# Optimization experiments

Measured on AMD Instinct MI355X. Metric: run time of the kernel, lower is better.

The kernel has to match this reference:

```python
import jax, jax.numpy as jnp
import numpy as np
import math

B, T, C = 4, 2048, 2048
HQ, HKV = 16, 4
HD = C // HQ          # 128
REP = HQ // HKV       # 4
EPS = 1e-6


def _rope_tables(seq_len, dim):
    inv_freq = 1.0 / (10000.0 ** (np.arange(0, dim, 2, dtype=np.float32) / dim))
    t = np.arange(seq_len, dtype=np.float32)
    freqs = np.einsum('i,j->ij', t, inv_freq)  # [T, dim/2]
    return jnp.asarray(np.cos(freqs)), jnp.asarray(np.sin(freqs))


def setup_inputs() -> dict:
    key = jax.random.key(0)
    ks = jax.random.split(key, 10)
    s = 0.02
    cos, sin = _rope_tables(T, HD)
    return {
        'x': jax.random.normal(ks[0], (B, T, C), jnp.float32),
        'Wq': jax.random.normal(ks[1], (C, C), jnp.float32) * s,
        'bq': jnp.zeros((C,), jnp.float32),
        'Wk': jax.random.normal(ks[2], (HD * HKV, C), jnp.float32) * s,
        'bk': jnp.zeros((HD * HKV,), jnp.float32),
        'Wv': jax.random.normal(ks[3], (HD * HKV, C), jnp.float32) * s,
        'bv': jnp.zeros((HD * HKV,), jnp.float32),
        'qn_w': jnp.ones((HD,), jnp.float32),
        'kn_w': jnp.ones((HD,), jnp.float32),
        'Wg': jax.random.normal(ks[4], (HD, HD), jnp.float32) * s,
        'bg': jnp.zeros((HD,), jnp.float32),
        'Wo': jax.random.normal(ks[5], (C, C), jnp.float32) * s,
        'bo': jnp.zeros((C,), jnp.float32),
        'cos': cos,
        'sin': sin,
    }


def _apply_rope(x, cos, sin):
    # x: [B,T,H,HD]; cos/sin: [T,HD/2]
    c = cos[None, :, None, :]
    s = sin[None, :, None, :]
    x1, x2 = x[..., ::2], x[..., 1::2]
    return jnp.concatenate([x1 * c - x2 * s, x1 * s + x2 * c], axis=-1)


def _rmsnorm(x, w):
    norm = jnp.mean(x * x, axis=-1, keepdims=True)
    return w * (x * jax.lax.rsqrt(norm + EPS))


def reference(x, Wq, bq, Wk, bk, Wv, bv, qn_w, kn_w, Wg, bg, Wo, bo, cos, sin):
    Bsz, Tlen, _ = x.shape
    q = (x @ Wq.T + bq).reshape(Bsz, Tlen, HQ, HD)
    k = (x @ Wk.T + bk).reshape(Bsz, Tlen, HKV, HD)
    v = (x @ Wv.T + bv).reshape(Bsz, Tlen, HKV, HD)

    q = _rmsnorm(_apply_rope(q, cos, sin), qn_w)
    k = _rmsnorm(_apply_rope(k, cos, sin), kn_w)

    # GQA without materializing repeated K/V: group q heads [B,T,HKV,REP,HD]
    # (repeat_interleave on kv-head dim matches this grouping exactly)
    q5 = q.reshape(Bsz, Tlen, HKV, REP, HD)
    scores = jnp.einsum('btkrd,bskd->bkrts', q5, k) / math.sqrt(HD)

    causal = jnp.tril(jnp.ones((Tlen, Tlen), bool))
    scores = jnp.where(causal, scores, -jnp.inf)
    probs = jax.nn.softmax(scores, axis=-1)

    out = jnp.einsum('bkrts,bskd->btkrd', probs, v).reshape(Bsz, Tlen, HQ, HD)
    gate = jax.nn.sigmoid(out @ Wg.T + bg)
    out = (out * gate).reshape(Bsz, Tlen, C)
    return out @ Wo.T + bo
```

## Files before the change

kernel.cpp:

```cpp
#include <hip/hip_runtime.h>
#include <hip/hip_bf16.h>
#include <math.h>

typedef __attribute__((ext_vector_type(8))) __bf16 bf16x8;
typedef __attribute__((ext_vector_type(4))) float f32x4;

__device__ __forceinline__ void stage16(const void* g, void* l) {
#if __has_builtin(__builtin_amdgcn_global_load_lds)
  __builtin_amdgcn_global_load_lds(
      (const __attribute__((address_space(1))) void*)g,
      (__attribute__((address_space(3))) void*)l, 16, 0, 0);
#else
  *(int4*)l = *(const int4*)g;
#endif
}

__device__ __forceinline__ float sigmoidf_(float x) {
  return 1.0f / (1.0f + __expf(-x));
}

__device__ __forceinline__ void f2b4(const float* __restrict__ s, __bf16* __restrict__ d) {
  float4 v = *(const float4*)s;
  union { __bf16 h[4]; int2 p; } u;
  u.h[0] = (__bf16)v.x; u.h[1] = (__bf16)v.y;
  u.h[2] = (__bf16)v.z; u.h[3] = (__bf16)v.w;
  *(int2*)d = u.p;
}

__global__ __launch_bounds__(256) void prep(const float* __restrict__ x,
                                            const float* __restrict__ Wq,
                                            const float* __restrict__ Wk,
                                            const float* __restrict__ Wv,
                                            const float* __restrict__ Wo,
                                            const float* __restrict__ Wg,
                                            const float* __restrict__ bq,
                                            const float* __restrict__ bk,
                                            const float* __restrict__ bv,
                                            __bf16* __restrict__ XB,
                                            __bf16* __restrict__ WQKVb,
                                            __bf16* __restrict__ WOb,
                                            __bf16* __restrict__ WGb,
                                            float* __restrict__ BQKV) {
  int c = blockIdx.x * 256 + threadIdx.x;
  if (c >= 6820608) return;
  if (c < 4194304) {
    f2b4(x + (size_t)c * 4, XB + (size_t)c * 4);
  } else if (c < 5242880) {
    int e = (c - 4194304) * 4;  f2b4(Wq + e, WQKVb + e);
  } else if (c < 5505024) {
    int e = (c - 5242880) * 4;  f2b4(Wk + e, WQKVb + 4194304 + e);
  } else if (c < 5767168) {
    int e = (c - 5505024) * 4;  f2b4(Wv + e, WQKVb + 5242880 + e);
  } else if (c < 6815744) {
    int e = (c - 5767168) * 4;  f2b4(Wo + e, WOb + e);
  } else if (c < 6819840) {
    int e = (c - 6815744) * 4;  f2b4(Wg + e, WGb + e);
  } else {
    int e = (c - 6819840) * 4;
    float4 v;
    if (e < 2048)      v = *(const float4*)(bq + e);
    else if (e < 2560) v = *(const float4*)(bk + (e - 2048));
    else               v = *(const float4*)(bv + (e - 2560));
    *(float4*)(BQKV + e) = v;
  }
}

template <typename OutT>
__global__ __launch_bounds__(512, 1) void gemm256(const __bf16* __restrict__ A,
                                                  const __bf16* __restrict__ Bm,
                                                  const float* __restrict__ bias,
                                                  OutT* __restrict__ C,
                                                  int M, int N, int K, int gx) {
  __shared__ __align__(16) __bf16 Sm[2][2][2][128 * 64];
  const int tid = threadIdx.x, lane = tid & 63, wid = tid >> 6;
  const int wm = wid >> 2, wn = wid & 3;
  const int r = lane & 15, g4 = lane >> 4;
  const int nwg = gridDim.x, qx = nwg >> 3;
  const int wg = (blockIdx.x & 7) * qx + (blockIdx.x >> 3);
  const int m0 = (wg / gx) * 256, n0 = (wg % gx) * 256;

  f32x4 acc[8][4] = {};
  const int NT = K >> 6;

#define STAGE_HALF(buf, which, half, kt)                                          \
  {                                                                               \
    const __bf16* sp_ = (which) ? Bm : A;                                         \
    const int base_ = ((which) ? n0 : m0) + (half) * 128;                         \
    const int k0_ = (kt) << 6;                                                    \
    __bf16* dp_ = &Sm[buf][which][half][0];                                       \
    _Pragma("unroll") for (int i_ = 0; i_ < 2; ++i_) {                            \
      int c_ = i_ * 512 + tid;                                                    \
      int row_ = c_ >> 3, slot_ = c_ & 7;                                         \
      stage16(sp_ + (size_t)(base_ + row_) * K + k0_ + ((slot_ ^ (row_ & 7)) << 3), \
              dp_ + c_ * 8);                                                      \
    }                                                                             \
  }
#define LDSW(base, row, kk) \
  (*(const bf16x8*)&(base)[(row) * 64 + ((((kk) * 4 + g4) ^ ((row) & 7)) << 3)])

  STAGE_HALF(0, 0, 0, 0) STAGE_HALF(0, 0, 1, 0) STAGE_HALF(0, 1, 0, 0) STAGE_HALF(0, 1, 1, 0)

  const int brow = (wn & 1) * 64;
  bf16x8 af[4][2], bfr[2][2];

  for (int kt = 0; kt < NT; ++kt) {
    const int cur = kt & 1, nxt = cur ^ 1;
    const bool more = (kt + 1) < NT;
    const __bf16* Ah = &Sm[cur][0][wm][0];
    const __bf16* Bh = &Sm[cur][1][wn >> 1][0];

    if (more) STAGE_HALF(nxt, 0, 0, kt + 1)
    if (more) { asm volatile("s_waitcnt vmcnt(2)" ::: "memory"); }
    else      { asm volatile("s_waitcnt vmcnt(0)" ::: "memory"); }
    __builtin_amdgcn_s_barrier();
    asm volatile("" ::: "memory");
#pragma unroll
    for (int m = 0; m < 4; ++m)
#pragma unroll
      for (int kk = 0; kk < 2; ++kk) af[m][kk] = LDSW(Ah, m * 16 + r, kk);
#pragma unroll
    for (int n = 0; n < 2; ++n)
#pragma unroll
      for (int kk = 0; kk < 2; ++kk) bfr[n][kk] = LDSW(Bh, brow + n * 16 + r, kk);
    asm volatile("s_waitcnt lgkmcnt(0)" ::: "memory");
    __builtin_amdgcn_sched_barrier(0);
    __builtin_amdgcn_s_setprio(1);
#pragma unroll
    for (int m = 0; m < 4; ++m)
#pragma unroll
      for (int n = 0; n < 2; ++n)
#pragma unroll
        for (int kk = 0; kk < 2; ++kk)
          acc[m][n] = __builtin_amdgcn_mfma_f32_16x16x32_bf16(af[m][kk], bfr[n][kk],
                                                              acc[m][n], 0, 0, 0);
    __builtin_amdgcn_s_setprio(0);
    __builtin_amdgcn_s_barrier();

#pragma unroll
    for (int n = 0; n < 2; ++n)
#pragma unroll
      for (int kk = 0; kk < 2; ++kk) bfr[n][kk] = LDSW(Bh, brow + (2 + n) * 16 + r, kk);
    if (more) STAGE_HALF(nxt, 0, 1, kt + 1)
    asm volatile("s_waitcnt lgkmcnt(0)" ::: "memory");
    __builtin_amdgcn_sched_barrier(0);
    __builtin_amdgcn_s_setprio(1);
#pragma unroll
    for (int m = 0; m < 4; ++m)
#pragma unroll
      for (int n = 0; n < 2; ++n)
#pragma unroll
        for (int kk = 0; kk < 2; ++kk)
          acc[m][2 + n] = __builtin_amdgcn_mfma_f32_16x16x32_bf16(af[m][kk], bfr[n][kk],
                                                                  acc[m][2 + n], 0, 0, 0);
    __builtin_amdgcn_s_setprio(0);
    __builtin_amdgcn_s_barrier();

#pragma unroll
    for (int m = 0; m < 4; ++m)
#pragma unroll
      for (int kk = 0; kk < 2; ++kk) af[m][kk] = LDSW(Ah, (4 + m) * 16 + r, kk);
#pragma unroll
    for (int n = 0; n < 2; ++n)
#pragma unroll
      for (int kk = 0; kk < 2; ++kk) bfr[n][kk] = LDSW(Bh, brow + n * 16 + r, kk);
    if (more) STAGE_HALF(nxt, 1, 0, kt + 1)
    asm volatile("s_waitcnt lgkmcnt(0)" ::: "memory");
    __builtin_amdgcn_sched_barrier(0);
    __builtin_amdgcn_s_setprio(1);
#pragma unroll
    for (int m = 0; m < 4; ++m)
#pragma unroll
      for (int n = 0; n < 2; ++n)
#pragma unroll
        for (int kk = 0; kk < 2; ++kk)
          acc[4 + m][n] = __builtin_amdgcn_mfma_f32_16x16x32_bf16(af[m][kk], bfr[n][kk],
                                                                  acc[4 + m][n], 0, 0, 0);
    __builtin_amdgcn_s_setprio(0);
    __builtin_amdgcn_s_barrier();

#pragma unroll
    for (int n = 0; n < 2; ++n)
#pragma unroll
      for (int kk = 0; kk < 2; ++kk) bfr[n][kk] = LDSW(Bh, brow + (2 + n) * 16 + r, kk);
    if (more) STAGE_HALF(nxt, 1, 1, kt + 1)
    asm volatile("s_waitcnt lgkmcnt(0)" ::: "memory");
    __builtin_amdgcn_sched_barrier(0);
    __builtin_amdgcn_s_setprio(1);
#pragma unroll
    for (int m = 0; m < 4; ++m)
#pragma unroll
      for (int n = 0; n < 2; ++n)
#pragma unroll
        for (int kk = 0; kk < 2; ++kk)
          acc[4 + m][2 + n] = __builtin_amdgcn_mfma_f32_16x16x32_bf16(af[m][kk], bfr[n][kk],
                                                                      acc[4 + m][2 + n], 0, 0, 0);
    __builtin_amdgcn_s_setprio(0);
    __builtin_amdgcn_s_barrier();
  }

  const int rq = lane >> 4;
#pragma unroll
  for (int m = 0; m < 8; ++m)
#pragma unroll
    for (int n = 0; n < 4; ++n) {
      int col = n0 + wn * 64 + n * 16 + r;
      float bv = bias ? bias[col] : 0.0f;
#pragma unroll
      for (int j = 0; j < 4; ++j) {
        int row = m0 + wm * 128 + m * 16 + rq * 4 + j;
        C[(size_t)row * N + col] = (OutT)(acc[m][n][j] + bv);
      }
    }
#undef STAGE_HALF
#undef LDSW
}

__global__ __launch_bounds__(512, 1) void gemm128(const __bf16* __restrict__ A,
                                                  const __bf16* __restrict__ Bm,
                                                  const float* __restrict__ bias,
                                                  __bf16* __restrict__ C,
                                                  int M, int N, int K, int gx) {
  __shared__ __align__(16) __bf16 Sm[2][3][128 * 64];
  const int tid = threadIdx.x, lane = tid & 63, wid = tid >> 6;
  const int wm = wid >> 2, wn = wid & 3;
  const int r = lane & 15, g4 = lane >> 4;
  const int nwg = gridDim.x, qx = nwg >> 3;
  const int wg = (blockIdx.x & 7) * qx + (blockIdx.x >> 3);
  const int m0 = (wg / gx) * 128, n0 = (wg % gx) * 256;

  f32x4 acc[4][4] = {};
  const int NT = K >> 6;

#define STAGE_SEG(buf, seg, sp, rowbase, kt)                                        \
  {                                                                                 \
    __bf16* dp_ = &Sm[buf][seg][0];                                                 \
    const int k0_ = (kt) << 6;                                                      \
    _Pragma("unroll") for (int i_ = 0; i_ < 2; ++i_) {                              \
      int c_ = i_ * 512 + tid;                                                      \
      int row_ = c_ >> 3, slot_ = c_ & 7;                                           \
      stage16((sp) + (size_t)((rowbase) + row_) * K + k0_ + ((slot_ ^ (row_ & 7)) << 3), \
              dp_ + c_ * 8);                                                        \
    }                                                                               \
  }
#define LDSW(base, row, kk) \
  (*(const bf16x8*)&(base)[(row) * 64 + ((((kk) * 4 + g4) ^ ((row) & 7)) << 3)])
#define MFMA8(nq)                                                                   \
  asm volatile("s_waitcnt lgkmcnt(0)" ::: "memory");                                \
  __builtin_amdgcn_sched_barrier(0);                                                \
  __builtin_amdgcn_s_setprio(1);                                                    \
  _Pragma("unroll") for (int m = 0; m < 4; ++m)                                     \
    _Pragma("unroll") for (int kk = 0; kk < 2; ++kk)                                \
      acc[m][nq] = __builtin_amdgcn_mfma_f32_16x16x32_bf16(af[m][kk], bfr[kk],      \
                                                           acc[m][nq], 0, 0, 0);    \
  __builtin_amdgcn_s_setprio(0);

  STAGE_SEG(0, 0, A, m0, 0) STAGE_SEG(0, 1, Bm, n0, 0) STAGE_SEG(0, 2, Bm, n0 + 128, 0)

  const int bseg = 1 + (wn >> 1);
  const int brow = (wn & 1) * 64;
  bf16x8 af[4][2], bfr[2];

  for (int kt = 0; kt < NT; ++kt) {
    const int cur = kt & 1, nxt = cur ^ 1;
    const bool more = (kt + 1) < NT;
    const __bf16* Ah = &Sm[cur][0][0];
    const __bf16* Bh = &Sm[cur][bseg][0];

    if (more) { STAGE_SEG(nxt, 0, A, m0, kt + 1)
                asm volatile("s_waitcnt vmcnt(2)" ::: "memory"); }
    else      { asm volatile("s_waitcnt vmcnt(0)" ::: "memory"); }
    __builtin_amdgcn_s_barrier();
    asm volatile("" ::: "memory");
#pragma unroll
    for (int m = 0; m < 4; ++m)
#pragma unroll
      for (int kk = 0; kk < 2; ++kk) af[m][kk] = LDSW(Ah, wm * 64 + m * 16 + r, kk);
#pragma unroll
    for (int kk = 0; kk < 2; ++kk) bfr[kk] = LDSW(Bh, brow + r, kk);
    MFMA8(0)

#pragma unroll
    for (int kk = 0; kk < 2; ++kk) bfr[kk] = LDSW(Bh, brow + 16 + r, kk);
    if (more) STAGE_SEG(nxt, 1, Bm, n0, kt + 1)
    MFMA8(1)

#pragma unroll
    for (int kk = 0; kk < 2; ++kk) bfr[kk] = LDSW(Bh, brow + 32 + r, kk);
    if (more) STAGE_SEG(nxt, 2, Bm, n0 + 128, kt + 1)
    MFMA8(2)

#pragma unroll
    for (int kk = 0; kk < 2; ++kk) bfr[kk] = LDSW(Bh, brow + 48 + r, kk);
    MFMA8(3)
    __builtin_amdgcn_s_barrier();
  }

  const int rq = lane >> 4;
#pragma unroll
  for (int m = 0; m < 4; ++m)
#pragma unroll
    for (int n = 0; n < 4; ++n) {
      int col = n0 + wn * 64 + n * 16 + r;
      float bv = bias ? bias[col] : 0.0f;
#pragma unroll
      for (int j = 0; j < 4; ++j) {
        int row = m0 + wm * 64 + m * 16 + rq * 4 + j;
        C[(size_t)row * N + col] = (__bf16)(acc[m][n][j] + bv);
      }
    }
#undef STAGE_SEG
#undef LDSW
#undef MFMA8
}

__global__ __launch_bounds__(256) void rope_vt(const __bf16* __restrict__ Y,
                                               const float* __restrict__ cosT,
                                               const float* __restrict__ sinT,
                                               const float* __restrict__ qn,
                                               const float* __restrict__ kn,
                                               __bf16* __restrict__ qat,
                                               __bf16* __restrict__ kat,
                                               __bf16* __restrict__ VT) {
  __shared__ __bf16 tile[32][66];
  if (blockIdx.x < 8192) {
    const int tok = blockIdx.x;
    const int b = tok >> 11, t = tok & 2047;
    const int wv = threadIdx.x >> 6, l = threadIdx.x & 63;
    const __bf16* row = Y + (size_t)tok * 3072;
    const float c = cosT[t * 64 + l], s = sinT[t * 64 + l];
    const float QS = 0.08838834764831845f * 1.4426950408889634f;
#pragma unroll
    for (int i = 0; i < 5; ++i) {
      const int h = wv + i * 4;
      const bool isq = h < 16;
      const int base = isq ? h * 128 : 2048 + (h - 16) * 128;
      union { uint32_t u; __bf16 h2[2]; } p;
      p.u = *(const uint32_t*)(row + base + 2 * l);
      float x1 = (float)p.h2[0], x2 = (float)p.h2[1];
      float v1 = x1 * c - x2 * s;
      float v2 = x1 * s + x2 * c;
      float ss = v1 * v1 + v2 * v2;
#pragma unroll
      for (int o = 32; o >= 1; o >>= 1) ss += __shfl_xor(ss, o, 64);
      float rms = rsqrtf(ss * (1.0f / 128.0f) + 1e-6f);
      if (isq) rms *= QS;
      float w1 = isq ? qn[l] : kn[l];
      float w2 = isq ? qn[64 + l] : kn[64 + l];
      size_t ob = isq ? (((size_t)b * 16 + h) * 2048 + t) * 128
                      : (((size_t)b * 4 + (h - 16)) * 2048 + t) * 128;
      __bf16* dst = isq ? qat : kat;
      dst[ob + l] = (__bf16)(w1 * v1 * rms);
      dst[ob + 64 + l] = (__bf16)(w2 * v2 * rms);
    }
  } else {
    const int i = blockIdx.x - 8192;
    const int t0 = (i & 31) * 64;
    const int d0 = ((i >> 5) & 3) * 32;
    const int bh = i >> 7;
    const int b = bh >> 2, hv = bh & 3;
    const __bf16* src = Y + (size_t)b * 2048 * 3072 + 2560 + hv * 128 + d0;
    const int dd = threadIdx.x & 31, tt = threadIdx.x >> 5;
#pragma unroll
    for (int p = 0; p < 8; ++p) {
      int t = tt + p * 8;
      tile[dd][t] = src[(size_t)(t0 + t) * 3072 + dd];
    }
    __syncthreads();
    __bf16* dst = VT + ((size_t)bh * 128 + d0) * 2048 + t0;
    const int oc = threadIdx.x & 63, orr = threadIdx.x >> 6;
#pragma unroll
    for (int p = 0; p < 8; ++p) {
      int d = orr + p * 4;
      dst[(size_t)d * 2048 + oc] = tile[d][oc];
    }
  }
}

__global__ __launch_bounds__(512, 4) void attn10(const __bf16* __restrict__ Q,
                                                 const __bf16* __restrict__ Kg,
                                                 const __bf16* __restrict__ VTg,
                                                 __bf16* __restrict__ ab) {
  __shared__ __align__(16) __bf16 Kt[2][64 * 128];
  __shared__ __align__(16) __bf16 Vt[2][128 * 64];
  __shared__ __align__(16) __bf16 Ps[8 * 16 * 64];
  const int tid = threadIdx.x, lane = tid & 63, wv = tid >> 6;
  const int L = blockIdx.x;
  const int xcd = L & 7, slot = L >> 3;
  const int group = xcd * 2 + (slot >> 5);
  const int idx = slot & 31;
  const int b = group >> 2, hkv = group & 3;
  const int hq = hkv * 4 + (idx >> 3);
  const int p = idx & 7;
  const __bf16* qp = Q + ((size_t)b * 16 + hq) * 2048 * 128;
  const __bf16* kp = Kg + ((size_t)b * 4 + hkv) * 2048 * 128;
  const __bf16* vp = VTg + ((size_t)b * 4 + hkv) * 128 * 2048;
  const int r = lane & 15, g4 = lane >> 4, ks = g4 * 8;

  bf16x8 vone;
#pragma unroll
  for (int e = 0; e < 8; ++e) vone[e] = (__bf16)1.0f;

#define STAGE_TILE(bi, kv0)                                                  \
  {                                                                          \
    __bf16* Kb = &Kt[bi][0];                                                 \
    __bf16* Vb = &Vt[bi][0];                                                 \
    _Pragma("unroll") for (int i = 0; i < 2; ++i) {                          \
      int c = i * 512 + tid;                                                 \
      int row = c >> 4, slot_ = c & 15;                                      \
      int gco = ((slot_ ^ (row & 7)) << 3);                                  \
      stage16(kp + (size_t)((kv0) + row) * 128 + gco, &Kb[c * 8]);           \
    }                                                                        \
    _Pragma("unroll") for (int i = 0; i < 2; ++i) {                          \
      int c = i * 512 + tid;                                                 \
      int row = c >> 3, slot_ = c & 7;                                       \
      int gco = ((slot_ ^ (row & 7)) << 3);                                  \
      stage16(vp + (size_t)row * 2048 + (kv0) + gco, &Vb[c * 8]);            \
    }                                                                        \
  }
#define SM_PAIR(k0)                                                          \
  _Pragma("unroll") for (int kj = (k0); kj < (k0) + 2; ++kj)                 \
    _Pragma("unroll") for (int j = 0; j < 4; ++j) {                          \
      float pv = exp2f(s[kj][j] - mrow[j]);                                  \
      int qr = g4 * 4 + j;                                                   \
      int kvl = kj * 16 + r;                                                 \
      int sl = (kvl >> 3) ^ (qr & 7);                                        \
      pw[qr * 64 + sl * 8 + (kvl & 7)] = (__bf16)pv;                         \
    }
#define PV_CHUNK(kvj)                                                        \
  {                                                                          \
    int sl = ((kvj) * 4 + g4) ^ (r & 7);                                     \
    bf16x8 pa = *(const bf16x8*)&pw[r * 64 + sl * 8];                        \
    __builtin_amdgcn_s_setprio(1);                                           \
    Lacc = __builtin_amdgcn_mfma_f32_16x16x32_bf16(pa, vone, Lacc, 0, 0, 0); \
    _Pragma("unroll") for (int dn = 0; dn < 8; ++dn) {                       \
      bf16x8 vb = *(const bf16x8*)&Vb[(dn * 16 + r) * 64 + sl * 8];          \
      Of[dn] = __builtin_amdgcn_mfma_f32_16x16x32_bf16(pa, vb, Of[dn], 0, 0, 0); \
    }                                                                        \
    __builtin_amdgcn_s_setprio(0);                                           \
  }

  for (int half = 0; half < 2; ++half) {
    const int qt = half == 0 ? (15 - p) : p;
    const int q0 = qt * 128 + wv * 16;

    bf16x8 qf[4];
#pragma unroll
    for (int kk = 0; kk < 4; ++kk)
      qf[kk] = *(const bf16x8*)(qp + (size_t)(q0 + r) * 128 + kk * 32 + ks);

    f32x4 Of[8] = {};
    f32x4 Lacc = {};
    float mrow[4] = {-1e30f, -1e30f, -1e30f, -1e30f};

    const int nt = 2 * qt + 2;
    STAGE_TILE(0, 0);
    int cur = 0;
    for (int t = 0; t < nt; ++t) {
      const int kv0 = t * 64;
      if (t + 1 < nt) {
        STAGE_TILE(cur ^ 1, (t + 1) * 64);
        asm volatile("s_waitcnt vmcnt(4)" ::: "memory");
      } else {
        asm volatile("s_waitcnt vmcnt(0)" ::: "memory");
      }
      __builtin_amdgcn_s_barrier();

      const __bf16* Kb = &Kt[cur][0];
      const __bf16* Vb = &Vt[cur][0];

      f32x4 s[4];
      __builtin_amdgcn_s_setprio(1);
#pragma unroll
      for (int kj = 0; kj < 4; ++kj) {
        f32x4 sa = {};
        int krow = kj * 16 + r;
#pragma unroll
        for (int kk = 0; kk < 4; ++kk) {
          int slot_ = (kk * 4 + g4) ^ (r & 7);
          bf16x8 kf = *(const bf16x8*)&Kb[krow * 128 + slot_ * 8];
          sa = __builtin_amdgcn_mfma_f32_16x16x32_bf16(qf[kk], kf, sa, 0, 0, 0);
        }
        s[kj] = sa;
      }
      __builtin_amdgcn_s_setprio(0);
      if (kv0 + 63 > q0) {
#pragma unroll
        for (int kj = 0; kj < 4; ++kj)
#pragma unroll
          for (int j = 0; j < 4; ++j) {
            int kv = kv0 + kj * 16 + r;
            int qrow = q0 + g4 * 4 + j;
            if (kv > qrow) s[kj][j] = -1e30f;
          }
      }
      float tm[4];
#pragma unroll
      for (int j = 0; j < 4; ++j)
        tm[j] = fmaxf(fmaxf(s[0][j], s[1][j]), fmaxf(s[2][j], s[3][j]));
      bool need = (tm[0] > mrow[0] + 8.0f) | (tm[1] > mrow[1] + 8.0f) |
                  (tm[2] > mrow[2] + 8.0f) | (tm[3] > mrow[3] + 8.0f);
      if (__any(need)) {
#pragma unroll
        for (int o = 8; o >= 1; o >>= 1)
#pragma unroll
          for (int j = 0; j < 4; ++j) tm[j] = fmaxf(tm[j], __shfl_xor(tm[j], o, 64));
#pragma unroll
        for (int j = 0; j < 4; ++j) {
          float mn = fmaxf(mrow[j], tm[j]);
          float corr = exp2f(mrow[j] - mn);
          mrow[j] = mn;
          Lacc[j] *= corr;
#pragma unroll
          for (int f = 0; f < 8; ++f) Of[f][j] *= corr;
        }
      }

      __bf16* pw = &Ps[wv * 16 * 64];
      SM_PAIR(0)
      PV_CHUNK(0)
      SM_PAIR(2)
      PV_CHUNK(1)
      __builtin_amdgcn_s_barrier();
      cur ^= 1;
    }

    float inv[4];
#pragma unroll
    for (int j = 0; j < 4; ++j) inv[j] = 1.0f / Lacc[j];
#pragma unroll
    for (int dn = 0; dn < 8; ++dn)
#pragma unroll
      for (int j = 0; j < 4; ++j) {
        int row = q0 + g4 * 4 + j;
        int d = dn * 16 + r;
        ab[(((size_t)b * 2048 + row) * 16 + hq) * 128 + d] = (__bf16)(Of[dn][j] * inv[j]);
      }
  }
#undef STAGE_TILE
#undef SM_PAIR
#undef PV_CHUNK
}

__global__ __launch_bounds__(256) void gate_fused(const __bf16* __restrict__ a,
                                                  const __bf16* __restrict__ WgB,
                                                  const float* __restrict__ bg,
                                                  __bf16* __restrict__ og) {
  __shared__ __align__(16) __bf16 Wl[128 * 128];
  const int tid = threadIdx.x, lane = tid & 63, wv = tid >> 6;
  const int r = lane & 15, g4 = lane >> 4, ks = g4 * 8;
#pragma unroll
  for (int i = 0; i < 8; ++i) {
    int c = i * 256 + tid;
    int row = c >> 4, slot = c & 15;
    *(bf16x8*)&Wl[row * 128 + ((slot ^ (row & 7)) << 3)] =
        *(const bf16x8*)&WgB[row * 128 + slot * 8];
  }
  __syncthreads();
  const size_t r0 = (size_t)blockIdx.x * 64 + wv * 16;
  bf16x8 af[4];
#pragma unroll
  for (int kk = 0; kk < 4; ++kk)
    af[kk] = *(const bf16x8*)(a + (r0 + r) * 128 + kk * 32 + ks);
  f32x4 acc[8] = {};
#pragma unroll
  for (int dn = 0; dn < 8; ++dn) {
    int row = dn * 16 + r;
#pragma unroll
    for (int kk = 0; kk < 4; ++kk) {
      bf16x8 bf_ = *(const bf16x8*)&Wl[row * 128 + (((kk * 4 + g4) ^ (row & 7)) << 3)];
      acc[dn] = __builtin_amdgcn_mfma_f32_16x16x32_bf16(af[kk], bf_, acc[dn], 0, 0, 0);
    }
  }
#pragma unroll
  for (int dn = 0; dn < 8; ++dn) {
    float bgv = bg[dn * 16 + r];
#pragma unroll
    for (int j = 0; j < 4; ++j) {
      size_t row = r0 + g4 * 4 + j;
      int col = dn * 16 + r;
      float gv = sigmoidf_(acc[dn][j] + bgv);
      float av = (float)a[row * 128 + col];
      og[row * 128 + col] = (__bf16)(av * gv);
    }
  }
}

extern "C" void kernel_launch(void* const* d_in, const int* in_sizes, int n_in,
                              void* d_out, int out_size, void* d_ws, size_t ws_size,
                              hipStream_t stream) {
  const float* x    = (const float*)d_in[0];
  const float* Wq   = (const float*)d_in[1];
  const float* bq   = (const float*)d_in[2];
  const float* Wk   = (const float*)d_in[3];
  const float* bk   = (const float*)d_in[4];
  const float* Wv   = (const float*)d_in[5];
  const float* bv   = (const float*)d_in[6];
  const float* qn   = (const float*)d_in[7];
  const float* kn   = (const float*)d_in[8];
  const float* Wg   = (const float*)d_in[9];
  const float* bg   = (const float*)d_in[10];
  const float* Wo   = (const float*)d_in[11];
  const float* bo   = (const float*)d_in[12];
  const float* cosT = (const float*)d_in[13];
  const float* sinT = (const float*)d_in[14];

  char* ws = (char*)d_ws;
  constexpr size_t OFF_WQKV = 0;
  constexpr size_t OFF_WO   = OFF_WQKV + 3072ull * 2048 * 2;
  constexpr size_t OFF_WG   = OFF_WO + 2048ull * 2048 * 2;
  constexpr size_t OFF_BQKV = OFF_WG + 128ull * 128 * 2;
  constexpr size_t OFF_XB   = OFF_BQKV + 16384;
  constexpr size_t OFF_Y    = OFF_XB + 8192ull * 2048 * 2;
  constexpr size_t OFF_QAT  = OFF_Y + 8192ull * 3072 * 2;
  constexpr size_t OFF_KAT  = OFF_QAT + 4ull * 16 * 2048 * 128 * 2;
  constexpr size_t OFF_VT   = OFF_KAT + 4ull * 4 * 2048 * 128 * 2;
  constexpr size_t OFF_AB   = OFF_VT + 4ull * 4 * 2048 * 128 * 2;

  __bf16* WQKVb = (__bf16*)(ws + OFF_WQKV);
  __bf16* WOb   = (__bf16*)(ws + OFF_WO);
  __bf16* WGb   = (__bf16*)(ws + OFF_WG);
  float*  BQKV  = (float*)(ws + OFF_BQKV);
  __bf16* XB    = (__bf16*)(ws + OFF_XB);
  __bf16* Y     = (__bf16*)(ws + OFF_Y);
  __bf16* QAT   = (__bf16*)(ws + OFF_QAT);
  __bf16* KAT   = (__bf16*)(ws + OFF_KAT);
  __bf16* VT    = (__bf16*)(ws + OFF_VT);
  __bf16* ABuf  = (__bf16*)(ws + OFF_AB);
  __bf16* OGB   = (__bf16*)(ws + OFF_XB);

  prep<<<26643, 256, 0, stream>>>(x, Wq, Wk, Wv, Wo, Wg, bq, bk, bv,
                                  XB, WQKVb, WOb, WGb, BQKV);

  gemm128<<<768, 512, 0, stream>>>(XB, WQKVb, BQKV, Y, 8192, 3072, 2048, 12);

  rope_vt<<<10240, 256, 0, stream>>>(Y, cosT, sinT, qn, kn, QAT, KAT, VT);

  attn10<<<512, 512, 0, stream>>>(QAT, KAT, VT, ABuf);

  gate_fused<<<2048, 256, 0, stream>>>(ABuf, WGb, bg, OGB);

  gemm256<float><<<256, 512, 0, stream>>>(OGB, WOb, bo, (float*)d_out, 8192, 2048, 2048, 8);
}
```

Before: 389.9 us.

## Process two 16-row query subtiles per wave in attention to reuse K/V fragments

The attention kernel drops from 8 waves to 4 waves per block, and each wave now handles 32 query rows as two 16-row subtiles instead of one. Each K and V fragment read from LDS then feeds two MFMAs, halving LDS read traffic per unit of compute. Each thread now issues twice as many staging loads, and the wait count is adjusted to match. The cost is roughly doubled accumulator and register use per wave and fewer waves per block, which may lower occupancy and latency hiding. The softmax interleaving between P writes and PV chunks is also simplified.

```diff
diff --git a/kernel.cpp b/kernel.cpp
--- a/kernel.cpp
+++ b/kernel.cpp
@@ -376,13 +376,13 @@
   }
 }
 
-__global__ __launch_bounds__(512, 4) void attn10(const __bf16* __restrict__ Q,
+__global__ __launch_bounds__(256, 2) void attn11(const __bf16* __restrict__ Q,
                                                  const __bf16* __restrict__ Kg,
                                                  const __bf16* __restrict__ VTg,
                                                  __bf16* __restrict__ ab) {
   __shared__ __align__(16) __bf16 Kt[2][64 * 128];
   __shared__ __align__(16) __bf16 Vt[2][128 * 64];
-  __shared__ __align__(16) __bf16 Ps[8 * 16 * 64];
+  __shared__ __align__(16) __bf16 Ps[4 * 32 * 64];
   const int tid = threadIdx.x, lane = tid & 63, wv = tid >> 6;
   const int L = blockIdx.x;
   const int xcd = L & 7, slot = L >> 3;
@@ -404,53 +404,35 @@
   {                                                                          \
     __bf16* Kb = &Kt[bi][0];                                                 \
     __bf16* Vb = &Vt[bi][0];                                                 \
-    _Pragma("unroll") for (int i = 0; i < 2; ++i) {                          \
-      int c = i * 512 + tid;                                                 \
+    _Pragma("unroll") for (int i = 0; i < 4; ++i) {                          \
+      int c = i * 256 + tid;                                                 \
       int row = c >> 4, slot_ = c & 15;                                      \
       int gco = ((slot_ ^ (row & 7)) << 3);                                  \
       stage16(kp + (size_t)((kv0) + row) * 128 + gco, &Kb[c * 8]);           \
     }                                                                        \
-    _Pragma("unroll") for (int i = 0; i < 2; ++i) {                          \
-      int c = i * 512 + tid;                                                 \
+    _Pragma("unroll") for (int i = 0; i < 4; ++i) {                          \
+      int c = i * 256 + tid;                                                 \
       int row = c >> 3, slot_ = c & 7;                                       \
       int gco = ((slot_ ^ (row & 7)) << 3);                                  \
       stage16(vp + (size_t)row * 2048 + (kv0) + gco, &Vb[c * 8]);            \
     }                                                                        \
   }
-#define SM_PAIR(k0)                                                          \
-  _Pragma("unroll") for (int kj = (k0); kj < (k0) + 2; ++kj)                 \
-    _Pragma("unroll") for (int j = 0; j < 4; ++j) {                          \
-      float pv = exp2f(s[kj][j] - mrow[j]);                                  \
-      int qr = g4 * 4 + j;                                                   \
-      int kvl = kj * 16 + r;                                                 \
-      int sl = (kvl >> 3) ^ (qr & 7);                                        \
-      pw[qr * 64 + sl * 8 + (kvl & 7)] = (__bf16)pv;                         \
-    }
-#define PV_CHUNK(kvj)                                                        \
-  {                                                                          \
-    int sl = ((kvj) * 4 + g4) ^ (r & 7);                                     \
-    bf16x8 pa = *(const bf16x8*)&pw[r * 64 + sl * 8];                        \
-    __builtin_amdgcn_s_setprio(1);                                           \
-    Lacc = __builtin_amdgcn_mfma_f32_16x16x32_bf16(pa, vone, Lacc, 0, 0, 0); \
-    _Pragma("unroll") for (int dn = 0; dn < 8; ++dn) {                       \
-      bf16x8 vb = *(const bf16x8*)&Vb[(dn * 16 + r) * 64 + sl * 8];          \
-      Of[dn] = __builtin_amdgcn_mfma_f32_16x16x32_bf16(pa, vb, Of[dn], 0, 0, 0); \
-    }                                                                        \
-    __builtin_amdgcn_s_setprio(0);                                           \
-  }
-
-  for (int half = 0; half < 2; ++half) {
-    const int qt = half == 0 ? (15 - p) : p;
-    const int q0 = qt * 128 + wv * 16;
-
-    bf16x8 qf[4];
-#pragma unroll
-    for (int kk = 0; kk < 4; ++kk)
-      qf[kk] = *(const bf16x8*)(qp + (size_t)(q0 + r) * 128 + kk * 32 + ks);
-
-    f32x4 Of[8] = {};
-    f32x4 Lacc = {};
-    float mrow[4] = {-1e30f, -1e30f, -1e30f, -1e30f};
+
+  for (int half_ = 0; half_ < 2; ++half_) {
+    const int qt = half_ == 0 ? (15 - p) : p;
+    const int q0 = qt * 128 + wv * 32;
+
+    bf16x8 qfA[4], qfB[4];
+#pragma unroll
+    for (int kk = 0; kk < 4; ++kk) {
+      qfA[kk] = *(const bf16x8*)(qp + (size_t)(q0 + r) * 128 + kk * 32 + ks);
+      qfB[kk] = *(const bf16x8*)(qp + (size_t)(q0 + 16 + r) * 128 + kk * 32 + ks);
+    }
+
+    f32x4 OfA[8] = {}, OfB[8] = {};
+    f32x4 LaccA = {}, LaccB = {};
+    float mrowA[4] = {-1e30f, -1e30f, -1e30f, -1e30f};
+    float mrowB[4] = {-1e30f, -1e30f, -1e30f, -1e30f};
 
     const int nt = 2 * qt + 2;
     STAGE_TILE(0, 0);
@@ -459,7 +441,7 @@
       const int kv0 = t * 64;
       if (t + 1 < nt) {
         STAGE_TILE(cur ^ 1, (t + 1) * 64);
-        asm volatile("s_waitcnt vmcnt(4)" ::: "memory");
+        asm volatile("s_waitcnt vmcnt(8)" ::: "memory");
       } else {
         asm volatile("s_waitcnt vmcnt(0)" ::: "memory");
       }
@@ -468,19 +450,20 @@
       const __bf16* Kb = &Kt[cur][0];
       const __bf16* Vb = &Vt[cur][0];
 
-      f32x4 s[4];
+      f32x4 sA[4], sB[4];
       __builtin_amdgcn_s_setprio(1);
 #pragma unroll
       for (int kj = 0; kj < 4; ++kj) {
-        f32x4 sa = {};
+        f32x4 saA = {}, saB = {};
         int krow = kj * 16 + r;
 #pragma unroll
         for (int kk = 0; kk < 4; ++kk) {
           int slot_ = (kk * 4 + g4) ^ (r & 7);
           bf16x8 kf = *(const bf16x8*)&Kb[krow * 128 + slot_ * 8];
-          sa = __builtin_amdgcn_mfma_f32_16x16x32_bf16(qf[kk], kf, sa, 0, 0, 0);
+          saA = __builtin_amdgcn_mfma_f32_16x16x32_bf16(qfA[kk], kf, saA, 0, 0, 0);
+          saB = __builtin_amdgcn_mfma_f32_16x16x32_bf16(qfB[kk], kf, saB, 0, 0, 0);
         }
-        s[kj] = sa;
+        sA[kj] = saA; sB[kj] = saB;
       }
       __builtin_amdgcn_s_setprio(0);
       if (kv0 + 63 > q0) {
@@ -489,56 +472,87 @@
 #pragma unroll
           for (int j = 0; j < 4; ++j) {
             int kv = kv0 + kj * 16 + r;
-            int qrow = q0 + g4 * 4 + j;
-            if (kv > qrow) s[kj][j] = -1e30f;
+            int qrA = q0 + g4 * 4 + j;
+            if (kv > qrA) sA[kj][j] = -1e30f;
+            if (kv > qrA + 16) sB[kj][j] = -1e30f;
           }
       }
-      float tm[4];
+      float tmA[4], tmB[4];
+#pragma unroll
+      for (int j = 0; j < 4; ++j) {
+        tmA[j] = fmaxf(fmaxf(sA[0][j], sA[1][j]), fmaxf(sA[2][j], sA[3][j]));
+        tmB[j] = fmaxf(fmaxf(sB[0][j], sB[1][j]), fmaxf(sB[2][j], sB[3][j]));
+      }
+      bool need = false;
 #pragma unroll
       for (int j = 0; j < 4; ++j)
-        tm[j] = fmaxf(fmaxf(s[0][j], s[1][j]), fmaxf(s[2][j], s[3][j]));
-      bool need = (tm[0] > mrow[0] + 8.0f) | (tm[1] > mrow[1] + 8.0f) |
-                  (tm[2] > mrow[2] + 8.0f) | (tm[3] > mrow[3] + 8.0f);
+        need |= (tmA[j] > mrowA[j] + 8.0f) | (tmB[j] > mrowB[j] + 8.0f);
       if (__any(need)) {
 #pragma unroll
         for (int o = 8; o >= 1; o >>= 1)
 #pragma unroll
-          for (int j = 0; j < 4; ++j) tm[j] = fmaxf(tm[j], __shfl_xor(tm[j], o, 64));
+          for (int j = 0; j < 4; ++j) {
+            tmA[j] = fmaxf(tmA[j], __shfl_xor(tmA[j], o, 64));
+            tmB[j] = fmaxf(tmB[j], __shfl_xor(tmB[j], o, 64));
+          }
 #pragma unroll
         for (int j = 0; j < 4; ++j) {
-          float mn = fmaxf(mrow[j], tm[j]);
-          float corr = exp2f(mrow[j] - mn);
-          mrow[j] = mn;
-          Lacc[j] *= corr;
-#pragma unroll
-          for (int f = 0; f < 8; ++f) Of[f][j] *= corr;
+          float mnA = fmaxf(mrowA[j], tmA[j]);
+          float cA = exp2f(mrowA[j] - mnA);
+          mrowA[j] = mnA; LaccA[j] *= cA;
+          float mnB = fmaxf(mrowB[j], tmB[j]);
+          float cB = exp2f(mrowB[j] - mnB);
+          mrowB[j] = mnB; LaccB[j] *= cB;
+#pragma unroll
+          for (int f = 0; f < 8; ++f) { OfA[f][j] *= cA; OfB[f][j] *= cB; }
         }
       }
-
-      __bf16* pw = &Ps[wv * 16 * 64];
-      SM_PAIR(0)
-      PV_CHUNK(0)
-      SM_PAIR(2)
-      PV_CHUNK(1)
+      __bf16* pw = &Ps[wv * 32 * 64];
+#pragma unroll
+      for (int kj = 0; kj < 4; ++kj)
+#pragma unroll
+        for (int j = 0; j < 4; ++j) {
+          int kvl = kj * 16 + r;
+          int qrA = g4 * 4 + j;
+          int slA = (kvl >> 3) ^ (qrA & 7);
+          pw[qrA * 64 + slA * 8 + (kvl & 7)] = (__bf16)exp2f(sA[kj][j] - mrowA[j]);
+          int qrB = 16 + qrA;
+          pw[qrB * 64 + slA * 8 + (kvl & 7)] = (__bf16)exp2f(sB[kj][j] - mrowB[j]);
+        }
+      __builtin_amdgcn_s_setprio(1);
+#pragma unroll
+      for (int kvj = 0; kvj < 2; ++kvj) {
+        int sl = (kvj * 4 + g4) ^ (r & 7);
+        bf16x8 paA = *(const bf16x8*)&pw[r * 64 + sl * 8];
+        bf16x8 paB = *(const bf16x8*)&pw[(16 + r) * 64 + sl * 8];
+        LaccA = __builtin_amdgcn_mfma_f32_16x16x32_bf16(paA, vone, LaccA, 0, 0, 0);
+        LaccB = __builtin_amdgcn_mfma_f32_16x16x32_bf16(paB, vone, LaccB, 0, 0, 0);
+#pragma unroll
+        for (int dn = 0; dn < 8; ++dn) {
+          bf16x8 vb = *(const bf16x8*)&Vb[(dn * 16 + r) * 64 + sl * 8];
+          OfA[dn] = __builtin_amdgcn_mfma_f32_16x16x32_bf16(paA, vb, OfA[dn], 0, 0, 0);
+          OfB[dn] = __builtin_amdgcn_mfma_f32_16x16x32_bf16(paB, vb, OfB[dn], 0, 0, 0);
+        }
+      }
+      __builtin_amdgcn_s_setprio(0);
       __builtin_amdgcn_s_barrier();
       cur ^= 1;
     }
 
-    float inv[4];
-#pragma unroll
-    for (int j = 0; j < 4; ++j) inv[j] = 1.0f / Lacc[j];
+    float invA[4], invB[4];
+#pragma unroll
+    for (int j = 0; j < 4; ++j) { invA[j] = 1.0f / LaccA[j]; invB[j] = 1.0f / LaccB[j]; }
 #pragma unroll
     for (int dn = 0; dn < 8; ++dn)
 #pragma unroll
       for (int j = 0; j < 4; ++j) {
-        int row = q0 + g4 * 4 + j;
+        int rowA = q0 + g4 * 4 + j;
         int d = dn * 16 + r;
-        ab[(((size_t)b * 2048 + row) * 16 + hq) * 128 + d] = (__bf16)(Of[dn][j] * inv[j]);
+        ab[(((size_t)b * 2048 + rowA) * 16 + hq) * 128 + d] = (__bf16)(OfA[dn][j] * invA[j]);
+        ab[(((size_t)b * 2048 + rowA + 16) * 16 + hq) * 128 + d] = (__bf16)(OfB[dn][j] * invB[j]);
       }
   }
 #undef STAGE_TILE
-#undef SM_PAIR
-#undef PV_CHUNK
 }
 
 __global__ __launch_bounds__(256) void gate_fused(const __bf16* __restrict__ a,
@@ -635,7 +649,7 @@
 
   rope_vt<<<10240, 256, 0, stream>>>(Y, cosT, sinT, qn, kn, QAT, KAT, VT);
 
-  attn10<<<512, 512, 0, stream>>>(QAT, KAT, VT, ABuf);
+  attn11<<<512, 256, 0, stream>>>(QAT, KAT, VT, ABuf);
 
   gate_fused<<<2048, 256, 0, stream>>>(ABuf, WGb, bg, OGB);
 
```

After: 384.9 us, median of 2. Within noise of the previous version (-1.3%).
